# Kernel tuning notes

Measured on AMD Instinct MI355X. Metric: run time of the kernel, lower is better.

## Reference

```python
import jax, jax.numpy as jnp
import numpy as np

B, NUM_CHUNKS, D_MODEL, L = 8, 1024, 512, 8192


def setup_inputs() -> dict:
    key = jax.random.key(0)
    k1, k2 = jax.random.split(key)
    compressed_x = jax.random.normal(k1, (B, NUM_CHUNKS, D_MODEL), dtype=jnp.float32)
    boundary_probs = jax.random.uniform(k2, (B, L), dtype=jnp.float32)
    return {"compressed_x": compressed_x, "boundary_probs": boundary_probs,
            "original_length": L}


def _expand(compressed_x, boundary_probs, original_length):
    """Boundary-indexed expansion, vectorized.

    Matches torch loop semantics:
      - position t is filled with chunk (k-1) where k = #boundaries at <= t,
        valid only when 1 <= k <= num_chunks; otherwise 0.
      - if a batch row has no boundaries, fall back to uniform chunking:
        chunk i fills [i*step, (i+1)*step), step = L // num_chunks.
    """
    batch, num_chunks, d_model = compressed_x.shape
    L_ = original_length
    mask = boundary_probs > 0.5                       # (B, L)
    cnt = jnp.cumsum(mask.astype(jnp.int32), axis=1)  # inclusive boundary count
    idx = jnp.clip(cnt - 1, 0, num_chunks - 1)        # chunk index per position
    valid = (cnt >= 1) & (cnt <= num_chunks)
    gathered = jnp.take_along_axis(compressed_x, idx[..., None], axis=1)  # (B, L, D)
    exp_b = jnp.where(valid[..., None], gathered, jnp.zeros((), gathered.dtype))

    # uniform fallback (no boundaries in the row)
    step = L_ // num_chunks
    t = jnp.arange(L_)
    u_idx = jnp.clip(t // step, 0, num_chunks - 1)    # (L,)
    u_valid = t < num_chunks * step                   # tail stays zero
    exp_u = jnp.where(u_valid[None, :, None], compressed_x[:, u_idx, :],
                      jnp.zeros((), compressed_x.dtype))

    has_b = mask.any(axis=1)                          # (B,)
    return jnp.where(has_b[:, None, None], exp_b, exp_u)


def _smooth(expanded, boundary_probs):
    """s[0]=e[0]; s[t] = a[t]*e[t] + (1-a[t])*s[t-1] via lax.scan over time."""
    e_t = jnp.swapaxes(expanded, 0, 1)                # (L, B, D)
    a_t = boundary_probs.T[:, :, None]                # (L, B, 1)

    def step_fn(s_prev, inp):
        a, e = inp
        s = a * e + (1.0 - a) * s_prev
        return s, s

    init = e_t[0]
    _, ys = jax.lax.scan(step_fn, init, (a_t[1:], e_t[1:]))
    out = jnp.concatenate([init[None], ys], axis=0)   # (L, B, D)
    return jnp.swapaxes(out, 0, 1)                    # (B, L, D)


def reference(compressed_x, boundary_probs, original_length):
    expanded = _expand(compressed_x, boundary_probs, original_length)
    return _smooth(expanded, boundary_probs)
```

## Files before the change

kernel.cpp:

```cpp
#include <hip/hip_runtime.h>

#define BB      8
#define LL      8192
#define DD      512
#define NCHUNK  1024
#define TC      64
#define NC      (LL/TC)

__global__ __launch_bounds__(256)
void k_index(const float* __restrict__ bp, int* __restrict__ idx_eff) {
    const int b   = blockIdx.x;
    const int tid = threadIdx.x;
    const int PER = LL / 256;
    const float* row = bp + (size_t)b * LL;
    const int base = tid * PER;

    int cnt_local = 0;
    for (int i = 0; i < PER; ++i)
        cnt_local += (row[base + i] > 0.5f) ? 1 : 0;

    __shared__ int s[256];
    s[tid] = cnt_local;
    __syncthreads();
    for (int off = 1; off < 256; off <<= 1) {
        int v = (tid >= off) ? s[tid - off] : 0;
        __syncthreads();
        s[tid] += v;
        __syncthreads();
    }
    const int excl  = (tid == 0) ? 0 : s[tid - 1];
    const int total = s[255];

    int* orow = idx_eff + (size_t)b * LL;
    if (total > 0) {
        int cnt = excl;
        for (int i = 0; i < PER; ++i) {
            const int t = base + i;
            cnt += (row[t] > 0.5f) ? 1 : 0;
            orow[t] = (cnt >= 1 && cnt <= NCHUNK) ? (cnt - 1) : -1;
        }
    } else {
        for (int i = 0; i < PER; ++i) {
            const int t = base + i;
            orow[t] = t >> 3;
        }
    }
}

__global__ __launch_bounds__(512)
void k_local(const float* __restrict__ cx, const float* __restrict__ bp,
             const int* __restrict__ idx_eff,
             float* __restrict__ Qend, float* __restrict__ Achunk) {
    const int blk = blockIdx.x;
    const int b = blk / NC, c = blk % NC;
    const int d = threadIdx.x;

    __shared__ float a_s[TC];
    __shared__ int   i_s[TC];
    if (d < TC) {
        const int t = c * TC + d;
        float a = bp[(size_t)b * LL + t];
        if (t == 0) a = 1.0f;
        a_s[d] = a;
        i_s[d] = idx_eff[(size_t)b * LL + t];
    }
    __syncthreads();

    const float* cxb = cx + (size_t)b * NCHUNK * DD;
    float q = 0.0f;
    for (int i = 0; i < TC; ++i) {
        const float a  = a_s[i];
        const int  idx = i_s[i];
        const float e  = (idx >= 0) ? cxb[(size_t)idx * DD + d] : 0.0f;
        q = a * e + (1.0f - a) * q;
    }
    Qend[((size_t)b * NC + c) * DD + d] = q;

    if (d == 0) {
        float P = 1.0f;
        for (int i = 0; i < TC; ++i) P *= (1.0f - a_s[i]);
        Achunk[b * NC + c] = P;
    }
}

__global__ __launch_bounds__(512)
void k_cross(const float* __restrict__ Qend, const float* __restrict__ Achunk,
             float* __restrict__ S0) {
    const int b = blockIdx.x;
    const int d = threadIdx.x;

    __shared__ float A_s[NC];
    if (d < NC) A_s[d] = Achunk[b * NC + d];
    __syncthreads();

    float s = 0.0f;
    for (int c = 0; c < NC; ++c) {
        const size_t o = ((size_t)b * NC + c) * DD + d;
        S0[o] = s;
        s = Qend[o] + A_s[c] * s;
    }
}

__global__ __launch_bounds__(512)
void k_final(const float* __restrict__ cx, const float* __restrict__ bp,
             const int* __restrict__ idx_eff, const float* __restrict__ S0,
             float* __restrict__ out) {
    const int blk = blockIdx.x;
    const int b = blk / NC, c = blk % NC;
    const int d = threadIdx.x;

    __shared__ float a_s[TC];
    __shared__ int   i_s[TC];
    if (d < TC) {
        const int t = c * TC + d;
        float a = bp[(size_t)b * LL + t];
        if (t == 0) a = 1.0f;
        a_s[d] = a;
        i_s[d] = idx_eff[(size_t)b * LL + t];
    }
    __syncthreads();

    const float* cxb = cx + (size_t)b * NCHUNK * DD;
    float s = S0[((size_t)b * NC + c) * DD + d];
    float* orow = out + ((size_t)b * LL + (size_t)c * TC) * DD + d;

    for (int i = 0; i < TC; ++i) {
        const float a  = a_s[i];
        const int  idx = i_s[i];
        const float e  = (idx >= 0) ? cxb[(size_t)idx * DD + d] : 0.0f;
        s = a * e + (1.0f - a) * s;
        orow[(size_t)i * DD] = s;
    }
}

extern "C" void kernel_launch(void* const* d_in, const int* in_sizes, int n_in,
                              void* d_out, int out_size, void* d_ws, size_t ws_size,
                              hipStream_t stream) {
    const float* cx = (const float*)d_in[0];
    const float* bp = (const float*)d_in[1];
    float* out = (float*)d_out;

    char* ws = (char*)d_ws;
    int*   idx_eff = (int*)(ws);
    float* Achunk  = (float*)(ws + 262144);
    float* Qend    = (float*)(ws + 266240);
    float* S0      = (float*)(ws + 2363392);

    k_index<<<BB,      256, 0, stream>>>(bp, idx_eff);
    k_local<<<BB * NC, 512, 0, stream>>>(cx, bp, idx_eff, Qend, Achunk);
    k_cross<<<BB,      512, 0, stream>>>(Qend, Achunk, S0);
    k_final<<<BB * NC, 512, 0, stream>>>(cx, bp, idx_eff, S0, out);
}
```

Before: 190.5 us.

## Fuse chunked scan into single-pass decoupled look-back kernel

Replaces the separate local-reduction, serial cross-chunk and final passes with one kernel that uses a ticket counter to order blocks, publishes each chunk's partial state and decay, and walks back over earlier chunks' published results with acquire/release flags, stopping once the decay factor reaches zero. This removes the serial k_cross pass and two kernel launches, plus the S0 round trip through memory. The index kernel is widened to 1024 threads with vectorized loads and stores, and it also resets the flags and ticket. The risks are spin-wait latency on chains of dependent blocks, and a look-back that can cost O(c) per block when the decay products stay nonzero.

```diff
diff --git a/kernel.cpp b/kernel.cpp
--- a/kernel.cpp
+++ b/kernel.cpp
@@ -7,127 +7,137 @@
 #define TC      64
 #define NC      (LL/TC)
 
-__global__ __launch_bounds__(256)
-void k_index(const float* __restrict__ bp, int* __restrict__ idx_eff) {
+__global__ __launch_bounds__(1024)
+void k_index(const float* __restrict__ bp, int* __restrict__ idx_eff,
+             int* __restrict__ flags, int* __restrict__ ticket) {
     const int b   = blockIdx.x;
     const int tid = threadIdx.x;
-    const int PER = LL / 256;
+
+    if (tid < NC) flags[b * NC + tid] = 0;
+    if (tid == 1023) *ticket = 0;
+
     const float* row = bp + (size_t)b * LL;
-    const int base = tid * PER;
+    const int base = tid * 8;
 
-    int cnt_local = 0;
-    for (int i = 0; i < PER; ++i)
-        cnt_local += (row[base + i] > 0.5f) ? 1 : 0;
+    float4 v0 = *reinterpret_cast<const float4*>(row + base);
+    float4 v1 = *reinterpret_cast<const float4*>(row + base + 4);
+    float pv[8] = {v0.x, v0.y, v0.z, v0.w, v1.x, v1.y, v1.z, v1.w};
 
-    __shared__ int s[256];
-    s[tid] = cnt_local;
+    int cl = 0;
+    #pragma unroll
+    for (int i = 0; i < 8; ++i) cl += (pv[i] > 0.5f) ? 1 : 0;
+
+    __shared__ int s[1024];
+    s[tid] = cl;
     __syncthreads();
-    for (int off = 1; off < 256; off <<= 1) {
+    #pragma unroll
+    for (int off = 1; off < 1024; off <<= 1) {
         int v = (tid >= off) ? s[tid - off] : 0;
         __syncthreads();
         s[tid] += v;
         __syncthreads();
     }
     const int excl  = (tid == 0) ? 0 : s[tid - 1];
-    const int total = s[255];
+    const int total = s[1023];
 
-    int* orow = idx_eff + (size_t)b * LL;
+    int out_i[8];
     if (total > 0) {
         int cnt = excl;
-        for (int i = 0; i < PER; ++i) {
-            const int t = base + i;
-            cnt += (row[t] > 0.5f) ? 1 : 0;
-            orow[t] = (cnt >= 1 && cnt <= NCHUNK) ? (cnt - 1) : -1;
+        #pragma unroll
+        for (int i = 0; i < 8; ++i) {
+            cnt += (pv[i] > 0.5f) ? 1 : 0;
+            out_i[i] = (cnt >= 1 && cnt <= NCHUNK) ? (cnt - 1) : -1;
         }
     } else {
-        for (int i = 0; i < PER; ++i) {
-            const int t = base + i;
-            orow[t] = t >> 3;
-        }
+        #pragma unroll
+        for (int i = 0; i < 8; ++i) out_i[i] = (base + i) >> 3;
     }
+    int* orow = idx_eff + (size_t)b * LL + base;
+    *reinterpret_cast<int4*>(orow)     = make_int4(out_i[0], out_i[1], out_i[2], out_i[3]);
+    *reinterpret_cast<int4*>(orow + 4) = make_int4(out_i[4], out_i[5], out_i[6], out_i[7]);
 }
 
 __global__ __launch_bounds__(512)
-void k_local(const float* __restrict__ cx, const float* __restrict__ bp,
-             const int* __restrict__ idx_eff,
-             float* __restrict__ Qend, float* __restrict__ Achunk) {
-    const int blk = blockIdx.x;
-    const int b = blk / NC, c = blk % NC;
-    const int d = threadIdx.x;
-
+void k_scan(const float* __restrict__ cx, const float* __restrict__ bp,
+            const int* __restrict__ idx_eff,
+            float* __restrict__ Qpub, float* __restrict__ Apub,
+            int* __restrict__ flags, int* __restrict__ ticket,
+            float* __restrict__ out) {
+    __shared__ int   sh_tk;
     __shared__ float a_s[TC];
     __shared__ int   i_s[TC];
-    if (d < TC) {
-        const int t = c * TC + d;
+    __shared__ float sh_A;
+
+    const int tid = threadIdx.x;
+    if (tid == 0) sh_tk = atomicAdd(ticket, 1);
+    __syncthreads();
+    const int tk = sh_tk;
+    const int b = tk >> 7;
+    const int c = tk & (NC - 1);
+
+    if (tid < TC) {
+        const int t = c * TC + tid;
         float a = bp[(size_t)b * LL + t];
         if (t == 0) a = 1.0f;
-        a_s[d] = a;
-        i_s[d] = idx_eff[(size_t)b * LL + t];
+        a_s[tid] = a;
+        i_s[tid] = idx_eff[(size_t)b * LL + t];
     }
     __syncthreads();
 
     const float* cxb = cx + (size_t)b * NCHUNK * DD;
+    const int d = tid;
+
     float q = 0.0f;
+    #pragma unroll 8
     for (int i = 0; i < TC; ++i) {
-        const float a  = a_s[i];
-        const int  idx = i_s[i];
-        const float e  = (idx >= 0) ? cxb[(size_t)idx * DD + d] : 0.0f;
+        const float a   = a_s[i];
+        const int   idx = i_s[i];
+        const float e   = (idx >= 0) ? cxb[(size_t)idx * DD + d] : 0.0f;
         q = a * e + (1.0f - a) * q;
     }
-    Qend[((size_t)b * NC + c) * DD + d] = q;
+    float A = 1.0f;
+    #pragma unroll 8
+    for (int i = 0; i < TC; ++i) A *= (1.0f - a_s[i]);
 
-    if (d == 0) {
-        float P = 1.0f;
-        for (int i = 0; i < TC; ++i) P *= (1.0f - a_s[i]);
-        Achunk[b * NC + c] = P;
+    const int slot = b * NC + c;
+    __hip_atomic_store(&Qpub[(size_t)slot * DD + d], q,
+                       __ATOMIC_RELAXED, __HIP_MEMORY_SCOPE_AGENT);
+    __threadfence();
+    __syncthreads();
+    if (tid == 0) {
+        __hip_atomic_store(&Apub[slot], A,
+                           __ATOMIC_RELAXED, __HIP_MEMORY_SCOPE_AGENT);
+        __hip_atomic_store(&flags[slot], 1,
+                           __ATOMIC_RELEASE, __HIP_MEMORY_SCOPE_AGENT);
     }
-}
 
-__global__ __launch_bounds__(512)
-void k_cross(const float* __restrict__ Qend, const float* __restrict__ Achunk,
-             float* __restrict__ S0) {
-    const int b = blockIdx.x;
-    const int d = threadIdx.x;
+    float prefix = 0.0f;
+    float factor = 1.0f;
+    for (int j = c - 1; j >= 0; --j) {
+        if (tid == 0) {
+            while (__hip_atomic_load(&flags[b * NC + j],
+                                     __ATOMIC_ACQUIRE, __HIP_MEMORY_SCOPE_AGENT) == 0) {
+                __builtin_amdgcn_s_sleep(4);
+            }
+            sh_A = __hip_atomic_load(&Apub[b * NC + j],
+                                     __ATOMIC_RELAXED, __HIP_MEMORY_SCOPE_AGENT);
+        }
+        __syncthreads();
+        const float qj = __hip_atomic_load(&Qpub[(size_t)(b * NC + j) * DD + d],
+                                           __ATOMIC_RELAXED, __HIP_MEMORY_SCOPE_AGENT);
+        prefix += factor * qj;
+        factor *= sh_A;
+        __syncthreads();
+        if (factor == 0.0f) break;
+    }
 
-    __shared__ float A_s[NC];
-    if (d < NC) A_s[d] = Achunk[b * NC + d];
-    __syncthreads();
-
-    float s = 0.0f;
-    for (int c = 0; c < NC; ++c) {
-        const size_t o = ((size_t)b * NC + c) * DD + d;
-        S0[o] = s;
-        s = Qend[o] + A_s[c] * s;
-    }
-}
-
-__global__ __launch_bounds__(512)
-void k_final(const float* __restrict__ cx, const float* __restrict__ bp,
-             const int* __restrict__ idx_eff, const float* __restrict__ S0,
-             float* __restrict__ out) {
-    const int blk = blockIdx.x;
-    const int b = blk / NC, c = blk % NC;
-    const int d = threadIdx.x;
-
-    __shared__ float a_s[TC];
-    __shared__ int   i_s[TC];
-    if (d < TC) {
-        const int t = c * TC + d;
-        float a = bp[(size_t)b * LL + t];
-        if (t == 0) a = 1.0f;
-        a_s[d] = a;
-        i_s[d] = idx_eff[(size_t)b * LL + t];
-    }
-    __syncthreads();
-
-    const float* cxb = cx + (size_t)b * NCHUNK * DD;
-    float s = S0[((size_t)b * NC + c) * DD + d];
+    float s = prefix;
     float* orow = out + ((size_t)b * LL + (size_t)c * TC) * DD + d;
-
+    #pragma unroll 8
     for (int i = 0; i < TC; ++i) {
-        const float a  = a_s[i];
-        const int  idx = i_s[i];
-        const float e  = (idx >= 0) ? cxb[(size_t)idx * DD + d] : 0.0f;
+        const float a   = a_s[i];
+        const int   idx = i_s[i];
+        const float e   = (idx >= 0) ? cxb[(size_t)idx * DD + d] : 0.0f;
         s = a * e + (1.0f - a) * s;
         orow[(size_t)i * DD] = s;
     }
@@ -142,12 +152,12 @@
 
     char* ws = (char*)d_ws;
     int*   idx_eff = (int*)(ws);
-    float* Achunk  = (float*)(ws + 262144);
-    float* Qend    = (float*)(ws + 266240);
-    float* S0      = (float*)(ws + 2363392);
+    int*   flags   = (int*)(ws + 262144);
+    float* Apub    = (float*)(ws + 266240);
+    int*   ticket  = (int*)(ws + 270336);
+    float* Qpub    = (float*)(ws + 274432);
 
-    k_index<<<BB,      256, 0, stream>>>(bp, idx_eff);
-    k_local<<<BB * NC, 512, 0, stream>>>(cx, bp, idx_eff, Qend, Achunk);
-    k_cross<<<BB,      512, 0, stream>>>(Qend, Achunk, S0);
-    k_final<<<BB * NC, 512, 0, stream>>>(cx, bp, idx_eff, S0, out);
+    k_index<<<BB,      1024, 0, stream>>>(bp, idx_eff, flags, ticket);
+    k_scan <<<BB * NC,  512, 0, stream>>>(cx, bp, idx_eff, Qpub, Apub,
+                                          flags, ticket, out);
 }
```

New measurement: 439.1 us. 130% more time.
